# Performance work log

Measured on AMD Instinct MI355X. Metric: run time of the kernel, lower is better.

Reference implementation:

```python
import jax, jax.numpy as jnp
import numpy as np


def setup_inputs() -> dict:
    key = jax.random.key(0)
    k1, k2, k3 = jax.random.split(key, 3)
    B, S, E = 4, 4096, 512
    x = jax.random.normal(k1, (B, S, E), dtype=jnp.float32)
    # xavier_uniform for Linear weights; zero biases (per _reset_parameters)
    lim_qkv = float(np.sqrt(6.0 / (E + 3 * E)))
    W_qkv = jax.random.uniform(k2, (3 * E, E), minval=-lim_qkv, maxval=lim_qkv, dtype=jnp.float32)
    b_qkv = jnp.zeros((3 * E,), dtype=jnp.float32)
    lim_out = float(np.sqrt(6.0 / (E + E)))
    W_out = jax.random.uniform(k3, (E, E), minval=-lim_out, maxval=lim_out, dtype=jnp.float32)
    b_out = jnp.zeros((E,), dtype=jnp.float32)
    return {"x": x, "W_qkv": W_qkv, "b_qkv": b_qkv, "W_out": W_out, "b_out": b_out}


def reference(x, W_qkv, b_qkv, W_out, b_out):
    B, S, E = x.shape
    H = 8
    D = E // H
    qkv = x @ W_qkv.T + b_qkv                      # [B,S,3E]
    qkv = qkv.reshape(B, S, H, 3 * D)
    q, k, v = jnp.split(qkv, 3, axis=-1)            # each [B,S,H,D]
    q = jax.nn.sigmoid(q)
    k = jax.nn.sigmoid(k)
    # flow conservation normalizers (sum over seq dim=1, then feature dim=3)
    i = jnp.sum(q * jnp.sum(k, axis=1, keepdims=True), axis=3, keepdims=True)      # [B,S,H,1]
    o = jnp.sum(k * jnp.sum(q, axis=1, keepdims=True), axis=3, keepdims=True)
    i_hat = jnp.sum(q * jnp.sum(k / o, axis=1, keepdims=True), axis=3, keepdims=True)
    o_hat = jnp.sum(k * jnp.sum(q / i, axis=1, keepdims=True), axis=3, keepdims=True)
    # NOTE: faithful to source — matmul batches over (B,S) and contracts the HEAD axis
    vw = v * jax.nn.softmax(o_hat, axis=1)          # [B,S,H,D]
    kv = jnp.einsum('bshd,bshe->bsde', k, vw)       # [B,S,D,D]
    r = jnp.einsum('bshd,bsde->bshe', q / i, kv) * jax.nn.sigmoid(i_hat)  # [B,S,H,D]
    values = r.reshape(B, S, E)
    return values @ W_out.T + b_out
```

## Files before the change

kernel.cpp:

```cpp
#include <hip/hip_runtime.h>
#include <cstdint>
#include <cstddef>

#define B_ 4
#define S_ 4096
#define E_ 512
#define NPOS 16384
#define QKVC 1536
#define K_ 512

typedef unsigned short u16;
typedef u16    u16x8  __attribute__((ext_vector_type(8)));
typedef u16    u16x4  __attribute__((ext_vector_type(4)));
typedef __bf16 bf16x8 __attribute__((ext_vector_type(8)));
typedef float  f32x4  __attribute__((ext_vector_type(4)));

__device__ __forceinline__ u16 f2bf(float f) {
    unsigned u = __builtin_bit_cast(unsigned, f);
    unsigned r = (u + 0x7fffu + ((u >> 16) & 1u)) >> 16;
    return (u16)r;
}
__device__ __forceinline__ float bf2f(u16 u) {
    return __builtin_bit_cast(float, (unsigned)u << 16);
}
__device__ __forceinline__ float rcpf(float x) { return __builtin_amdgcn_rcpf(x); }

__device__ __forceinline__ void async16(const void* g, void* lds) {
    __builtin_amdgcn_global_load_lds(
        (const __attribute__((address_space(1))) unsigned int*)g,
        (__attribute__((address_space(3))) unsigned int*)lds, 16, 0, 0);
}

__global__ __launch_bounds__(256) void cvt3(
        const float4* __restrict__ x, const float4* __restrict__ wq, const float4* __restrict__ wo,
        u16x4* __restrict__ ox, u16x4* __restrict__ owq, u16x4* __restrict__ owo) {
    const int n1 = NPOS * E_ / 4, n2 = QKVC * E_ / 4, n3 = E_ * E_ / 4;
    int i = blockIdx.x * 256 + threadIdx.x;
    const float4* in; u16x4* out; int j;
    if (i < n1)            { in = x;  out = ox;  j = i; }
    else if (i < n1 + n2)  { in = wq; out = owq; j = i - n1; }
    else if (i < n1+n2+n3) { in = wo; out = owo; j = i - n1 - n2; }
    else return;
    float4 v = in[j];
    u16x4 o;
    o[0] = f2bf(v.x); o[1] = f2bf(v.y); o[2] = f2bf(v.z); o[3] = f2bf(v.w);
    out[j] = o;
}

__global__ __launch_bounds__(256) void gemm_qkv(
        const u16* __restrict__ A, const u16* __restrict__ Bw,
        const float* __restrict__ bias,
        u16* __restrict__ Qb, u16* __restrict__ Kb, u16* __restrict__ Vb,
        int K) {
    __shared__ u16 As[128 * 32];
    __shared__ u16 Bs[128 * 32];
    const int tid  = threadIdx.x;
    const int wave = tid >> 6, lane = tid & 63;
    const int m0 = blockIdx.y * 128, n0 = blockIdx.x * 128;
    const int wm = (wave & 1) * 64, wn = (wave >> 1) * 64;

    const int srow = wave * 16 + (lane >> 2);
    const int scol = (lane & 3) * 8;
    const u16* Ap = A  + (size_t)(m0 + srow) * K + scol;
    const u16* Bp = Bw + (size_t)(n0 + srow) * K + scol;
    u16* AsW = &As[wave * 512];
    u16* BsW = &Bs[wave * 512];
    const size_t rstep = (size_t)64 * K;

    f32x4 acc[4][4] = {};
    const int fr = lane & 15, fk = (lane >> 4) * 8;

    for (int k0 = 0; k0 < K; k0 += 32) {
        async16(Ap + k0,         AsW);
        async16(Ap + k0 + rstep, AsW + 2048);
        async16(Bp + k0,         BsW);
        async16(Bp + k0 + rstep, BsW + 2048);
        __syncthreads();
        bf16x8 a[4], b[4];
        #pragma unroll
        for (int i = 0; i < 4; ++i)
            a[i] = *(const bf16x8*)&As[(wm + i * 16 + fr) * 32 + fk];
        #pragma unroll
        for (int j = 0; j < 4; ++j)
            b[j] = *(const bf16x8*)&Bs[(wn + j * 16 + fr) * 32 + fk];
        #pragma unroll
        for (int i = 0; i < 4; ++i)
            #pragma unroll
            for (int j = 0; j < 4; ++j)
                acc[i][j] = __builtin_amdgcn_mfma_f32_16x16x32_bf16(a[i], b[j], acc[i][j], 0, 0, 0);
        __syncthreads();
    }

    const int cn = lane & 15, rb = (lane >> 4) * 4;
    const int cg   = (n0 + wn) >> 6;
    const int type = cg % 3;
    const int hb   = cg / 3;
    u16* dst = (type == 0) ? Qb : (type == 1) ? Kb : Vb;
    const bool sg = (type < 2);
    #pragma unroll
    for (int i = 0; i < 4; ++i) {
        int mbase = m0 + wm + i * 16 + rb;
        #pragma unroll
        for (int j = 0; j < 4; ++j) {
            int ccol = j * 16 + cn;
            float bv = bias[n0 + wn + ccol];
            int outcol = hb * 64 + ccol;
            f32x4 av = acc[i][j];
            #pragma unroll
            for (int r = 0; r < 4; ++r) {
                float v = av[r] + bv;
                if (sg) v = 1.f / (1.f + __expf(-v));
                dst[(size_t)(mbase + r) * 512 + outcol] = f2bf(v);
            }
        }
    }
}

__global__ __launch_bounds__(256) void gemm_out(
        const u16* __restrict__ A, const u16* __restrict__ Bw,
        const float* __restrict__ bias, float* __restrict__ C,
        int N, int K) {
    __shared__ u16 As[128 * 32];
    __shared__ u16 Bs[128 * 32];
    const int tid  = threadIdx.x;
    const int wave = tid >> 6, lane = tid & 63;
    const int m0 = blockIdx.y * 128, n0 = blockIdx.x * 128;
    const int wm = (wave & 1) * 64, wn = (wave >> 1) * 64;
    const int srow = wave * 16 + (lane >> 2);
    const int scol = (lane & 3) * 8;
    const u16* Ap = A  + (size_t)(m0 + srow) * K + scol;
    const u16* Bp = Bw + (size_t)(n0 + srow) * K + scol;
    u16* AsW = &As[wave * 512];
    u16* BsW = &Bs[wave * 512];
    const size_t rstep = (size_t)64 * K;
    f32x4 acc[4][4] = {};
    const int fr = lane & 15, fk = (lane >> 4) * 8;
    for (int k0 = 0; k0 < K; k0 += 32) {
        async16(Ap + k0,         AsW);
        async16(Ap + k0 + rstep, AsW + 2048);
        async16(Bp + k0,         BsW);
        async16(Bp + k0 + rstep, BsW + 2048);
        __syncthreads();
        bf16x8 a[4], b[4];
        #pragma unroll
        for (int i = 0; i < 4; ++i)
            a[i] = *(const bf16x8*)&As[(wm + i * 16 + fr) * 32 + fk];
        #pragma unroll
        for (int j = 0; j < 4; ++j)
            b[j] = *(const bf16x8*)&Bs[(wn + j * 16 + fr) * 32 + fk];
        #pragma unroll
        for (int i = 0; i < 4; ++i)
            #pragma unroll
            for (int j = 0; j < 4; ++j)
                acc[i][j] = __builtin_amdgcn_mfma_f32_16x16x32_bf16(a[i], b[j], acc[i][j], 0, 0, 0);
        __syncthreads();
    }
    const int cn = lane & 15, rb = (lane >> 4) * 4;
    #pragma unroll
    for (int i = 0; i < 4; ++i) {
        int mbase = m0 + wm + i * 16 + rb;
        #pragma unroll
        for (int j = 0; j < 4; ++j) {
            int nn = n0 + wn + j * 16 + cn;
            float bv = bias[nn];
            f32x4 av = acc[i][j];
            #pragma unroll
            for (int r = 0; r < 4; ++r)
                C[(size_t)(mbase + r) * N + nn] = av[r] + bv;
        }
    }
}

__global__ __launch_bounds__(256, 4) void sum_qk(
        const u16* __restrict__ Qg, const u16* __restrict__ Kg,
        float* __restrict__ part) {
    __shared__ float red[4][1024];
    const int blk = blockIdx.x;
    const int b = blk >> 8, chunk = blk & 255;
    const int w = threadIdx.x >> 6, lane = threadIdx.x & 63;
    const int p0 = b * S_ + chunk * 16 + w * 4;
    float aq[8] = {}, ak[8] = {};
    #pragma unroll
    for (int it = 0; it < 4; ++it) {
        size_t off = (size_t)(p0 + it) * 512 + lane * 8;
        u16x8 q8 = *(const u16x8*)(Qg + off);
        u16x8 k8 = *(const u16x8*)(Kg + off);
        #pragma unroll
        for (int j = 0; j < 8; ++j) { aq[j] += bf2f(q8[j]); ak[j] += bf2f(k8[j]); }
    }
    #pragma unroll
    for (int j = 0; j < 8; ++j) {
        red[w][lane * 8 + j]       = aq[j];
        red[w][512 + lane * 8 + j] = ak[j];
    }
    __syncthreads();
    const int tid = threadIdx.x;
    float* dst = part + (size_t)blk * 1024;
    #pragma unroll
    for (int rr = 0; rr < 4; ++rr) {
        int slot = rr * 256 + tid;
        dst[slot] = red[0][slot] + red[1][slot] + red[2][slot] + red[3][slot];
    }
}

__global__ __launch_bounds__(256) void fold_qk(
        const float* __restrict__ part, float* __restrict__ sumq, float* __restrict__ sumk) {
    int t = blockIdx.x * 256 + threadIdx.x;
    int b = t >> 10, slot = t & 1023;
    float a = 0.f;
    const float* p = part + (size_t)b * 256 * 1024 + slot;
    for (int c = 0; c < 256; ++c) a += p[(size_t)c * 1024];
    if (slot < 512) sumq[b * 512 + slot] = a;
    else            sumk[b * 512 + (slot - 512)] = a;
}

__global__ __launch_bounds__(256, 4) void p2_io(
        const u16* __restrict__ Qg, const u16* __restrict__ Kg,
        const float* __restrict__ sumq, const float* __restrict__ sumk,
        float* __restrict__ iv, float* __restrict__ part) {
    __shared__ float red[4][1024];
    const int blk = blockIdx.x;
    const int b = blk >> 9, chunk = blk & 511;
    const int w = threadIdx.x >> 6, lane = threadIdx.x & 63;
    const int p0 = b * S_ + chunk * 8 + w * 2;
    float skL[8], sqL[8];
    #pragma unroll
    for (int j = 0; j < 8; ++j) {
        skL[j] = sumk[b * 512 + lane * 8 + j];
        sqL[j] = sumq[b * 512 + lane * 8 + j];
    }
    float aqi[8] = {}, ako[8] = {};
    #pragma unroll
    for (int it = 0; it < 2; ++it) {
        int p = p0 + it;
        size_t off = (size_t)p * 512 + lane * 8;
        u16x8 q8 = *(const u16x8*)(Qg + off);
        u16x8 k8 = *(const u16x8*)(Kg + off);
        float qf[8], kf[8];
        #pragma unroll
        for (int j = 0; j < 8; ++j) { qf[j] = bf2f(q8[j]); kf[j] = bf2f(k8[j]); }
        float di = 0.f, dox = 0.f;
        #pragma unroll
        for (int j = 0; j < 8; ++j) { di += qf[j] * skL[j]; dox += kf[j] * sqL[j]; }
        di  += __shfl_xor(di, 1);  di  += __shfl_xor(di, 2);  di  += __shfl_xor(di, 4);
        dox += __shfl_xor(dox, 1); dox += __shfl_xor(dox, 2); dox += __shfl_xor(dox, 4);
        if ((lane & 7) == 0) iv[(size_t)p * 8 + (lane >> 3)] = di;
        float ri = rcpf(di), ro = rcpf(dox);
        #pragma unroll
        for (int j = 0; j < 8; ++j) { aqi[j] += qf[j] * ri; ako[j] += kf[j] * ro; }
    }
    #pragma unroll
    for (int j = 0; j < 8; ++j) {
        red[w][lane * 8 + j]       = aqi[j];
        red[w][512 + lane * 8 + j] = ako[j];
    }
    __syncthreads();
    const int tid = threadIdx.x;
    float* dst = part + (size_t)blk * 1024;
    #pragma unroll
    for (int rr = 0; rr < 4; ++rr) {
        int slot = rr * 256 + tid;
        dst[slot] = red[0][slot] + red[1][slot] + red[2][slot] + red[3][slot];
    }
}

__global__ __launch_bounds__(256) void fold_io(
        const float* __restrict__ part, float* __restrict__ sumqi, float* __restrict__ sumko) {
    int t = blockIdx.x * 256 + threadIdx.x;
    int b = t >> 10, slot = t & 1023;
    float a = 0.f;
    const float* p = part + (size_t)b * 512 * 1024 + slot;
    for (int c = 0; c < 512; ++c) a += p[(size_t)c * 1024];
    if (slot < 512) sumqi[b * 512 + slot] = a;
    else            sumko[b * 512 + (slot - 512)] = a;
}

__global__ __launch_bounds__(256, 4) void p3_io2(
        const u16* __restrict__ Qg, const u16* __restrict__ Kg,
        const float* __restrict__ sumqi, const float* __restrict__ sumko,
        const float* __restrict__ iv,
        float* __restrict__ rsc, float* __restrict__ wexp, float* __restrict__ smpart) {
    __shared__ float smr[4][8];
    const int blk = blockIdx.x;
    const int b = blk >> 9, chunk = blk & 511;
    const int w = threadIdx.x >> 6, lane = threadIdx.x & 63;
    const int p0 = b * S_ + chunk * 8 + w * 2;
    float skoL[8], sqiL[8];
    #pragma unroll
    for (int j = 0; j < 8; ++j) {
        skoL[j] = sumko[b * 512 + lane * 8 + j];
        sqiL[j] = sumqi[b * 512 + lane * 8 + j];
    }
    float smacc = 0.f;
    #pragma unroll
    for (int it = 0; it < 2; ++it) {
        int p = p0 + it;
        size_t off = (size_t)p * 512 + lane * 8;
        u16x8 q8 = *(const u16x8*)(Qg + off);
        u16x8 k8 = *(const u16x8*)(Kg + off);
        float dih = 0.f, doh = 0.f;
        #pragma unroll
        for (int j = 0; j < 8; ++j) {
            dih += bf2f(q8[j]) * skoL[j];
            doh += bf2f(k8[j]) * sqiL[j];
        }
        dih += __shfl_xor(dih, 1); dih += __shfl_xor(dih, 2); dih += __shfl_xor(dih, 4);
        doh += __shfl_xor(doh, 1); doh += __shfl_xor(doh, 2); doh += __shfl_xor(doh, 4);
        if ((lane & 7) == 0) {
            int h = lane >> 3;
            float sig = 1.f / (1.f + __expf(-dih));
            rsc[(size_t)p * 8 + h] = sig * rcpf(iv[(size_t)p * 8 + h]);
            float we = __expf(fminf(doh, 80.f));
            wexp[(size_t)p * 8 + h] = we;
            smacc += we;
        }
    }
    if ((lane & 7) == 0) smr[w][lane >> 3] = smacc;
    __syncthreads();
    if (threadIdx.x < 8)
        smpart[(size_t)blk * 8 + threadIdx.x] =
            smr[0][threadIdx.x] + smr[1][threadIdx.x] + smr[2][threadIdx.x] + smr[3][threadIdx.x];
}

__global__ __launch_bounds__(256) void fold_sm(const float* __restrict__ smpart, float* __restrict__ sm) {
    __shared__ float red[256];
    int bh = blockIdx.x;
    int b = bh >> 3, h = bh & 7;
    float a = 0.f;
    for (int c = threadIdx.x; c < 512; c += 256)
        a += smpart[((size_t)b * 512 + c) * 8 + h];
    red[threadIdx.x] = a;
    __syncthreads();
    for (int st = 128; st > 0; st >>= 1) {
        if (threadIdx.x < st) red[threadIdx.x] += red[threadIdx.x + st];
        __syncthreads();
    }
    if (threadIdx.x == 0) sm[bh] = red[0];
}

__global__ __launch_bounds__(256) void finalize_kernel(
        const u16* __restrict__ Qg, const u16* __restrict__ Kg, const u16* __restrict__ Vg,
        const float* __restrict__ rsc, const float* __restrict__ wexp, const float* __restrict__ sm,
        u16* __restrict__ Rg) {
    __shared__ float Ml[4][2][8][9];
    __shared__ float vw[4][2][8][68];
    const int w = threadIdx.x >> 6, lane = threadIdx.x & 63;
    const int pp = blockIdx.x * 8 + w * 2;
    const int b = pp >> 12;

    {
        int pl = (lane >> 3) & 1, hh = lane & 7, quad = lane >> 4;
        const u16* qa = Qg + (size_t)(pp + pl) * 512 + hh * 64 + quad * 8;
        const u16* ka = Kg + (size_t)(pp + pl) * 512 + hh * 64 + quad * 8;
        bf16x8 a0 = __builtin_bit_cast(bf16x8, *(const u16x8*)qa);
        bf16x8 a1 = __builtin_bit_cast(bf16x8, *(const u16x8*)(qa + 32));
        bf16x8 b0 = __builtin_bit_cast(bf16x8, *(const u16x8*)ka);
        bf16x8 b1 = __builtin_bit_cast(bf16x8, *(const u16x8*)(ka + 32));
        f32x4 accm = {0.f, 0.f, 0.f, 0.f};
        accm = __builtin_amdgcn_mfma_f32_16x16x32_bf16(a0, b0, accm, 0, 0, 0);
        accm = __builtin_amdgcn_mfma_f32_16x16x32_bf16(a1, b1, accm, 0, 0, 0);
        if (((lane >> 5) & 1) == ((lane >> 3) & 1)) {
            int plm = lane >> 5, hr = ((lane >> 4) & 1) * 4, h2 = lane & 7;
            #pragma unroll
            for (int r = 0; r < 4; ++r)
                Ml[w][plm][hr + r][h2] = accm[r] * rsc[(size_t)(pp + plm) * 8 + hr + r];
        }
    }
    {
        int hv = lane >> 3, e0 = (lane & 7) * 8;
        float invsm = rcpf(sm[b * 8 + hv]);
        #pragma unroll
        for (int pl = 0; pl < 2; ++pl) {
            u16x8 v8 = *(const u16x8*)(Vg + (size_t)(pp + pl) * 512 + lane * 8);
            float wgt = wexp[(size_t)(pp + pl) * 8 + hv] * invsm;
            f32x4 x0, x1;
            #pragma unroll
            for (int j = 0; j < 4; ++j) { x0[j] = bf2f(v8[j]) * wgt; x1[j] = bf2f(v8[4 + j]) * wgt; }
            *(f32x4*)&vw[w][pl][hv][e0]     = x0;
            *(f32x4*)&vw[w][pl][hv][e0 + 4] = x1;
        }
    }
    __syncthreads();
    {
        int pl = lane >> 5, idx = lane & 31, h = idx >> 2, eq = (idx & 3) * 16;
        float outv[16] = {};
        #pragma unroll
        for (int h2 = 0; h2 < 8; ++h2) {
            float m = Ml[w][pl][h][h2];
            #pragma unroll
            for (int c = 0; c < 4; ++c) {
                f32x4 vv = *(const f32x4*)&vw[w][pl][h2][eq + c * 4];
                #pragma unroll
                for (int j = 0; j < 4; ++j) outv[c * 4 + j] += m * vv[j];
            }
        }
        u16x8 o0, o1;
        #pragma unroll
        for (int j = 0; j < 8; ++j) { o0[j] = f2bf(outv[j]); o1[j] = f2bf(outv[8 + j]); }
        u16* dstp = Rg + (size_t)(pp + pl) * 512 + h * 64 + eq;
        *(u16x8*)dstp       = o0;
        *(u16x8*)(dstp + 8) = o1;
    }
}

extern "C" void kernel_launch(void* const* d_in, const int* in_sizes, int n_in,
                              void* d_out, int out_size, void* d_ws, size_t ws_size,
                              hipStream_t stream) {
    const float* x    = (const float*)d_in[0];
    const float* Wqkv = (const float*)d_in[1];
    const float* bqkv = (const float*)d_in[2];
    const float* Wout = (const float*)d_in[3];
    const float* bout = (const float*)d_in[4];
    float* out = (float*)d_out;
    char* ws = (char*)d_ws;

    constexpr size_t SZ_XBF  = (size_t)NPOS * E_ * 2;
    constexpr size_t SZ_WQBF = (size_t)QKVC * E_ * 2;
    constexpr size_t SZ_WOBF = (size_t)E_ * E_ * 2;
    constexpr size_t SZ_QKVB = (size_t)NPOS * E_ * 2;
    constexpr size_t SZ_SUM  = (size_t)B_ * 512 * 4;
    constexpr size_t SZ_V8   = (size_t)NPOS * 8 * 4;
    constexpr size_t SZ_PART = (size_t)2048 * 1024 * 4;

    size_t off = 0;
    u16*   xbf    = (u16*)(ws + off);   off += SZ_XBF;
    u16*   wqbf   = (u16*)(ws + off);   off += SZ_WQBF;
    u16*   wobf   = (u16*)(ws + off);   off += SZ_WOBF;
    u16*   Qb     = (u16*)(ws + off);   off += SZ_QKVB;
    u16*   Kb     = (u16*)(ws + off);   off += SZ_QKVB;
    u16*   Vb     = (u16*)(ws + off);   off += SZ_QKVB;
    float* sumq   = (float*)(ws + off); off += SZ_SUM;
    float* sumk   = (float*)(ws + off); off += SZ_SUM;
    float* sumqi  = (float*)(ws + off); off += SZ_SUM;
    float* sumko  = (float*)(ws + off); off += SZ_SUM;
    float* sm     = (float*)(ws + off); off += 256;
    float* iv     = (float*)(ws + off); off += SZ_V8;
    float* rsc    = (float*)(ws + off); off += SZ_V8;
    float* wexp   = (float*)(ws + off); off += SZ_V8;
    float* smpart = (float*)(ws + off); off += (size_t)2048 * 8 * 4;
    float* part   = (float*)(ws + off); off += SZ_PART;
    u16*   rbf    = xbf;

    {
        const int n4 = (NPOS * E_ + QKVC * E_ + E_ * E_) / 4;
        cvt3<<<(n4 + 255) / 256, 256, 0, stream>>>(
            (const float4*)x, (const float4*)Wqkv, (const float4*)Wout,
            (u16x4*)xbf, (u16x4*)wqbf, (u16x4*)wobf);
    }

    gemm_qkv<<<dim3(QKVC / 128, NPOS / 128), 256, 0, stream>>>(
        xbf, wqbf, bqkv, Qb, Kb, Vb, K_);

    sum_qk<<<1024, 256, 0, stream>>>(Qb, Kb, part);
    fold_qk<<<16, 256, 0, stream>>>(part, sumq, sumk);

    p2_io<<<2048, 256, 0, stream>>>(Qb, Kb, sumq, sumk, iv, part);
    fold_io<<<16, 256, 0, stream>>>(part, sumqi, sumko);

    p3_io2<<<2048, 256, 0, stream>>>(Qb, Kb, sumqi, sumko, iv, rsc, wexp, smpart);
    fold_sm<<<32, 256, 0, stream>>>(smpart, sm);

    finalize_kernel<<<2048, 256, 0, stream>>>(Qb, Kb, Vb, rsc, wexp, sm, rbf);

    gemm_out<<<dim3(E_ / 128, NPOS / 128), 256, 0, stream>>>(
        rbf, wobf, bout, out, E_, K_);
}
```

Baseline: 226.2 us.

## Fuse Q/K column sums into QKV GEMM epilogue and move i_hat into finalize

The QKV GEMM epilogue now reduces the sigmoid outputs per column and writes per-tile partial sums, and a small fold kernel replaces the separate sum_qk pass that re-read Q and K. The i_hat dot product and sigmoid scaling move into the finalize kernel, so p3 only reads K and the rsc buffer is dropped. LDS reads in both GEMMs use an XOR swizzle to cut bank conflicts, and fold_io spreads its reduction over more blocks. The costs are extra epilogue work and a block barrier in the GEMM, plus some added arithmetic in finalize.

```diff
diff --git a/kernel.cpp b/kernel.cpp
--- a/kernel.cpp
+++ b/kernel.cpp
@@ -51,16 +51,18 @@
         const u16* __restrict__ A, const u16* __restrict__ Bw,
         const float* __restrict__ bias,
         u16* __restrict__ Qb, u16* __restrict__ Kb, u16* __restrict__ Vb,
+        float* __restrict__ pgem,
         int K) {
     __shared__ u16 As[128 * 32];
     __shared__ u16 Bs[128 * 32];
+    __shared__ float csums[2][2][64];
     const int tid  = threadIdx.x;
     const int wave = tid >> 6, lane = tid & 63;
     const int m0 = blockIdx.y * 128, n0 = blockIdx.x * 128;
     const int wm = (wave & 1) * 64, wn = (wave >> 1) * 64;
 
     const int srow = wave * 16 + (lane >> 2);
-    const int scol = (lane & 3) * 8;
+    const int scol = (((lane & 3) ^ ((lane >> 2) & 3))) * 8;
     const u16* Ap = A  + (size_t)(m0 + srow) * K + scol;
     const u16* Bp = Bw + (size_t)(n0 + srow) * K + scol;
     u16* AsW = &As[wave * 512];
@@ -68,7 +70,8 @@
     const size_t rstep = (size_t)64 * K;
 
     f32x4 acc[4][4] = {};
-    const int fr = lane & 15, fk = (lane >> 4) * 8;
+    const int fr = lane & 15, fq = lane >> 4;
+    const int fkA = ((fq ^ (fr & 3))) * 8;
 
     for (int k0 = 0; k0 < K; k0 += 32) {
         async16(Ap + k0,         AsW);
@@ -79,10 +82,10 @@
         bf16x8 a[4], b[4];
         #pragma unroll
         for (int i = 0; i < 4; ++i)
-            a[i] = *(const bf16x8*)&As[(wm + i * 16 + fr) * 32 + fk];
+            a[i] = *(const bf16x8*)&As[(wm + i * 16 + fr) * 32 + fkA];
         #pragma unroll
         for (int j = 0; j < 4; ++j)
-            b[j] = *(const bf16x8*)&Bs[(wn + j * 16 + fr) * 32 + fk];
+            b[j] = *(const bf16x8*)&Bs[(wn + j * 16 + fr) * 32 + fkA];
         #pragma unroll
         for (int i = 0; i < 4; ++i)
             #pragma unroll
@@ -97,22 +100,56 @@
     const int hb   = cg / 3;
     u16* dst = (type == 0) ? Qb : (type == 1) ? Kb : Vb;
     const bool sg = (type < 2);
-    #pragma unroll
-    for (int i = 0; i < 4; ++i) {
-        int mbase = m0 + wm + i * 16 + rb;
-        #pragma unroll
-        for (int j = 0; j < 4; ++j) {
-            int ccol = j * 16 + cn;
-            float bv = bias[n0 + wn + ccol];
-            int outcol = hb * 64 + ccol;
+    float col4[4];
+    #pragma unroll
+    for (int j = 0; j < 4; ++j) {
+        int ccol = j * 16 + cn;
+        float bv = bias[n0 + wn + ccol];
+        int outcol = hb * 64 + ccol;
+        float csum = 0.f;
+        #pragma unroll
+        for (int i = 0; i < 4; ++i) {
+            int mbase = m0 + wm + i * 16 + rb;
             f32x4 av = acc[i][j];
             #pragma unroll
             for (int r = 0; r < 4; ++r) {
                 float v = av[r] + bv;
                 if (sg) v = 1.f / (1.f + __expf(-v));
+                csum += v;
                 dst[(size_t)(mbase + r) * 512 + outcol] = f2bf(v);
             }
         }
+        csum += __shfl_xor(csum, 16);
+        csum += __shfl_xor(csum, 32);
+        col4[j] = csum;
+    }
+    if (lane < 16) {
+        #pragma unroll
+        for (int j = 0; j < 4; ++j)
+            csums[wave >> 1][wave & 1][j * 16 + lane] = col4[j];
+    }
+    __syncthreads();
+    if (tid < 128) {
+        int half = tid >> 6, c6 = tid & 63;
+        float s = csums[half][0][c6] + csums[half][1][c6];
+        int cgb = blockIdx.x * 2 + half;
+        pgem[((size_t)cgb * 128 + blockIdx.y) * 64 + c6] = s;
+    }
+}
+
+__global__ __launch_bounds__(256) void fold_gemm(
+        const float* __restrict__ pgem, float* __restrict__ sumq, float* __restrict__ sumk) {
+    int type = blockIdx.x >> 2, b = blockIdx.x & 3;
+    float* dst = (type == 0) ? sumq : sumk;
+    #pragma unroll
+    for (int rep = 0; rep < 2; ++rep) {
+        int col = rep * 256 + threadIdx.x;
+        int hbq = col >> 6, c6 = col & 63;
+        int cg = hbq * 3 + type;
+        float a = 0.f;
+        for (int mt = 0; mt < 32; ++mt)
+            a += pgem[((size_t)cg * 128 + b * 32 + mt) * 64 + c6];
+        dst[b * 512 + col] = a;
     }
 }
 
@@ -127,14 +164,15 @@
     const int m0 = blockIdx.y * 128, n0 = blockIdx.x * 128;
     const int wm = (wave & 1) * 64, wn = (wave >> 1) * 64;
     const int srow = wave * 16 + (lane >> 2);
-    const int scol = (lane & 3) * 8;
+    const int scol = (((lane & 3) ^ ((lane >> 2) & 3))) * 8;
     const u16* Ap = A  + (size_t)(m0 + srow) * K + scol;
     const u16* Bp = Bw + (size_t)(n0 + srow) * K + scol;
     u16* AsW = &As[wave * 512];
     u16* BsW = &Bs[wave * 512];
     const size_t rstep = (size_t)64 * K;
     f32x4 acc[4][4] = {};
-    const int fr = lane & 15, fk = (lane >> 4) * 8;
+    const int fr = lane & 15, fq = lane >> 4;
+    const int fkA = ((fq ^ (fr & 3))) * 8;
     for (int k0 = 0; k0 < K; k0 += 32) {
         async16(Ap + k0,         AsW);
         async16(Ap + k0 + rstep, AsW + 2048);
@@ -144,10 +182,10 @@
         bf16x8 a[4], b[4];
         #pragma unroll
         for (int i = 0; i < 4; ++i)
-            a[i] = *(const bf16x8*)&As[(wm + i * 16 + fr) * 32 + fk];
+            a[i] = *(const bf16x8*)&As[(wm + i * 16 + fr) * 32 + fkA];
         #pragma unroll
         for (int j = 0; j < 4; ++j)
-            b[j] = *(const bf16x8*)&Bs[(wn + j * 16 + fr) * 32 + fk];
+            b[j] = *(const bf16x8*)&Bs[(wn + j * 16 + fr) * 32 + fkA];
         #pragma unroll
         for (int i = 0; i < 4; ++i)
             #pragma unroll
@@ -169,49 +207,6 @@
                 C[(size_t)(mbase + r) * N + nn] = av[r] + bv;
         }
     }
-}
-
-__global__ __launch_bounds__(256, 4) void sum_qk(
-        const u16* __restrict__ Qg, const u16* __restrict__ Kg,
-        float* __restrict__ part) {
-    __shared__ float red[4][1024];
-    const int blk = blockIdx.x;
-    const int b = blk >> 8, chunk = blk & 255;
-    const int w = threadIdx.x >> 6, lane = threadIdx.x & 63;
-    const int p0 = b * S_ + chunk * 16 + w * 4;
-    float aq[8] = {}, ak[8] = {};
-    #pragma unroll
-    for (int it = 0; it < 4; ++it) {
-        size_t off = (size_t)(p0 + it) * 512 + lane * 8;
-        u16x8 q8 = *(const u16x8*)(Qg + off);
-        u16x8 k8 = *(const u16x8*)(Kg + off);
-        #pragma unroll
-        for (int j = 0; j < 8; ++j) { aq[j] += bf2f(q8[j]); ak[j] += bf2f(k8[j]); }
-    }
-    #pragma unroll
-    for (int j = 0; j < 8; ++j) {
-        red[w][lane * 8 + j]       = aq[j];
-        red[w][512 + lane * 8 + j] = ak[j];
-    }
-    __syncthreads();
-    const int tid = threadIdx.x;
-    float* dst = part + (size_t)blk * 1024;
-    #pragma unroll
-    for (int rr = 0; rr < 4; ++rr) {
-        int slot = rr * 256 + tid;
-        dst[slot] = red[0][slot] + red[1][slot] + red[2][slot] + red[3][slot];
-    }
-}
-
-__global__ __launch_bounds__(256) void fold_qk(
-        const float* __restrict__ part, float* __restrict__ sumq, float* __restrict__ sumk) {
-    int t = blockIdx.x * 256 + threadIdx.x;
-    int b = t >> 10, slot = t & 1023;
-    float a = 0.f;
-    const float* p = part + (size_t)b * 256 * 1024 + slot;
-    for (int c = 0; c < 256; ++c) a += p[(size_t)c * 1024];
-    if (slot < 512) sumq[b * 512 + slot] = a;
-    else            sumk[b * 512 + (slot - 512)] = a;
 }
 
 __global__ __launch_bounds__(256, 4) void p2_io(
@@ -266,52 +261,47 @@
 
 __global__ __launch_bounds__(256) void fold_io(
         const float* __restrict__ part, float* __restrict__ sumqi, float* __restrict__ sumko) {
-    int t = blockIdx.x * 256 + threadIdx.x;
-    int b = t >> 10, slot = t & 1023;
+    __shared__ float red[4][64];
+    const int b = blockIdx.x >> 4, sgrp = blockIdx.x & 15;
+    const int sub = threadIdx.x >> 6, lane = threadIdx.x & 63;
     float a = 0.f;
-    const float* p = part + (size_t)b * 512 * 1024 + slot;
-    for (int c = 0; c < 512; ++c) a += p[(size_t)c * 1024];
-    if (slot < 512) sumqi[b * 512 + slot] = a;
-    else            sumko[b * 512 + (slot - 512)] = a;
-}
-
-__global__ __launch_bounds__(256, 4) void p3_io2(
-        const u16* __restrict__ Qg, const u16* __restrict__ Kg,
-        const float* __restrict__ sumqi, const float* __restrict__ sumko,
-        const float* __restrict__ iv,
-        float* __restrict__ rsc, float* __restrict__ wexp, float* __restrict__ smpart) {
+    for (int i = 0; i < 128; ++i) {
+        int c = sub + i * 4;
+        a += part[((size_t)(b * 512 + c)) * 1024 + sgrp * 64 + lane];
+    }
+    red[sub][lane] = a;
+    __syncthreads();
+    if (threadIdx.x < 64) {
+        float s = red[0][lane] + red[1][lane] + red[2][lane] + red[3][lane];
+        int slot = sgrp * 64 + lane;
+        if (slot < 512) sumqi[b * 512 + slot] = s;
+        else            sumko[b * 512 + (slot - 512)] = s;
+    }
+}
+
+__global__ __launch_bounds__(256, 4) void p3_ohat(
+        const u16* __restrict__ Kg, const float* __restrict__ sumqi,
+        float* __restrict__ wexp, float* __restrict__ smpart) {
     __shared__ float smr[4][8];
     const int blk = blockIdx.x;
     const int b = blk >> 9, chunk = blk & 511;
     const int w = threadIdx.x >> 6, lane = threadIdx.x & 63;
     const int p0 = b * S_ + chunk * 8 + w * 2;
-    float skoL[8], sqiL[8];
-    #pragma unroll
-    for (int j = 0; j < 8; ++j) {
-        skoL[j] = sumko[b * 512 + lane * 8 + j];
-        sqiL[j] = sumqi[b * 512 + lane * 8 + j];
-    }
+    float sqiL[8];
+    #pragma unroll
+    for (int j = 0; j < 8; ++j) sqiL[j] = sumqi[b * 512 + lane * 8 + j];
     float smacc = 0.f;
     #pragma unroll
     for (int it = 0; it < 2; ++it) {
         int p = p0 + it;
-        size_t off = (size_t)p * 512 + lane * 8;
-        u16x8 q8 = *(const u16x8*)(Qg + off);
-        u16x8 k8 = *(const u16x8*)(Kg + off);
-        float dih = 0.f, doh = 0.f;
-        #pragma unroll
-        for (int j = 0; j < 8; ++j) {
-            dih += bf2f(q8[j]) * skoL[j];
-            doh += bf2f(k8[j]) * sqiL[j];
-        }
-        dih += __shfl_xor(dih, 1); dih += __shfl_xor(dih, 2); dih += __shfl_xor(dih, 4);
+        u16x8 k8 = *(const u16x8*)(Kg + (size_t)p * 512 + lane * 8);
+        float doh = 0.f;
+        #pragma unroll
+        for (int j = 0; j < 8; ++j) doh += bf2f(k8[j]) * sqiL[j];
         doh += __shfl_xor(doh, 1); doh += __shfl_xor(doh, 2); doh += __shfl_xor(doh, 4);
         if ((lane & 7) == 0) {
-            int h = lane >> 3;
-            float sig = 1.f / (1.f + __expf(-dih));
-            rsc[(size_t)p * 8 + h] = sig * rcpf(iv[(size_t)p * 8 + h]);
             float we = __expf(fminf(doh, 80.f));
-            wexp[(size_t)p * 8 + h] = we;
+            wexp[(size_t)p * 8 + (lane >> 3)] = we;
             smacc += we;
         }
     }
@@ -340,7 +330,8 @@
 
 __global__ __launch_bounds__(256) void finalize_kernel(
         const u16* __restrict__ Qg, const u16* __restrict__ Kg, const u16* __restrict__ Vg,
-        const float* __restrict__ rsc, const float* __restrict__ wexp, const float* __restrict__ sm,
+        const float* __restrict__ sumko, const float* __restrict__ iv,
+        const float* __restrict__ wexp, const float* __restrict__ sm,
         u16* __restrict__ Rg) {
     __shared__ float Ml[4][2][8][9];
     __shared__ float vw[4][2][8][68];
@@ -348,48 +339,61 @@
     const int pp = blockIdx.x * 8 + w * 2;
     const int b = pp >> 12;
 
-    {
-        int pl = (lane >> 3) & 1, hh = lane & 7, quad = lane >> 4;
-        const u16* qa = Qg + (size_t)(pp + pl) * 512 + hh * 64 + quad * 8;
-        const u16* ka = Kg + (size_t)(pp + pl) * 512 + hh * 64 + quad * 8;
-        bf16x8 a0 = __builtin_bit_cast(bf16x8, *(const u16x8*)qa);
-        bf16x8 a1 = __builtin_bit_cast(bf16x8, *(const u16x8*)(qa + 32));
-        bf16x8 b0 = __builtin_bit_cast(bf16x8, *(const u16x8*)ka);
-        bf16x8 b1 = __builtin_bit_cast(bf16x8, *(const u16x8*)(ka + 32));
-        f32x4 accm = {0.f, 0.f, 0.f, 0.f};
-        accm = __builtin_amdgcn_mfma_f32_16x16x32_bf16(a0, b0, accm, 0, 0, 0);
-        accm = __builtin_amdgcn_mfma_f32_16x16x32_bf16(a1, b1, accm, 0, 0, 0);
-        if (((lane >> 5) & 1) == ((lane >> 3) & 1)) {
-            int plm = lane >> 5, hr = ((lane >> 4) & 1) * 4, h2 = lane & 7;
-            #pragma unroll
-            for (int r = 0; r < 4; ++r)
-                Ml[w][plm][hr + r][h2] = accm[r] * rsc[(size_t)(pp + plm) * 8 + hr + r];
-        }
+    const int pl = (lane >> 3) & 1, hh = lane & 7, quad = lane >> 4;
+    const u16* qa = Qg + (size_t)(pp + pl) * 512 + hh * 64 + quad * 8;
+    const u16* ka = Kg + (size_t)(pp + pl) * 512 + hh * 64 + quad * 8;
+    u16x8 qv0 = *(const u16x8*)qa;
+    u16x8 qv1 = *(const u16x8*)(qa + 32);
+    bf16x8 b0 = __builtin_bit_cast(bf16x8, *(const u16x8*)ka);
+    bf16x8 b1 = __builtin_bit_cast(bf16x8, *(const u16x8*)(ka + 32));
+    f32x4 accm = {0.f, 0.f, 0.f, 0.f};
+    accm = __builtin_amdgcn_mfma_f32_16x16x32_bf16(__builtin_bit_cast(bf16x8, qv0), b0, accm, 0, 0, 0);
+    accm = __builtin_amdgcn_mfma_f32_16x16x32_bf16(__builtin_bit_cast(bf16x8, qv1), b1, accm, 0, 0, 0);
+
+    const float* sko = sumko + b * 512 + hh * 64 + quad * 8;
+    float dp = 0.f;
+    #pragma unroll
+    for (int j = 0; j < 8; ++j)
+        dp += bf2f(qv0[j]) * sko[j] + bf2f(qv1[j]) * sko[32 + j];
+    dp += __shfl_xor(dp, 16);
+    dp += __shfl_xor(dp, 32);
+    float sig = 1.f / (1.f + __expf(-dp));
+    float myrsc = sig * rcpf(iv[(size_t)(pp + pl) * 8 + hh]);
+
+    const int plm = lane >> 5, hr = ((lane >> 4) & 1) * 4, h2c = lane & 7;
+    float rsc4[4];
+    #pragma unroll
+    for (int r = 0; r < 4; ++r)
+        rsc4[r] = __shfl(myrsc, plm * 8 + hr + r);
+    if (((lane >> 5) & 1) == ((lane >> 3) & 1)) {
+        #pragma unroll
+        for (int r = 0; r < 4; ++r)
+            Ml[w][plm][hr + r][h2c] = accm[r] * rsc4[r];
     }
     {
         int hv = lane >> 3, e0 = (lane & 7) * 8;
         float invsm = rcpf(sm[b * 8 + hv]);
         #pragma unroll
-        for (int pl = 0; pl < 2; ++pl) {
-            u16x8 v8 = *(const u16x8*)(Vg + (size_t)(pp + pl) * 512 + lane * 8);
-            float wgt = wexp[(size_t)(pp + pl) * 8 + hv] * invsm;
+        for (int plv = 0; plv < 2; ++plv) {
+            u16x8 v8 = *(const u16x8*)(Vg + (size_t)(pp + plv) * 512 + lane * 8);
+            float wgt = wexp[(size_t)(pp + plv) * 8 + hv] * invsm;
             f32x4 x0, x1;
             #pragma unroll
             for (int j = 0; j < 4; ++j) { x0[j] = bf2f(v8[j]) * wgt; x1[j] = bf2f(v8[4 + j]) * wgt; }
-            *(f32x4*)&vw[w][pl][hv][e0]     = x0;
-            *(f32x4*)&vw[w][pl][hv][e0 + 4] = x1;
+            *(f32x4*)&vw[w][plv][hv][e0]     = x0;
+            *(f32x4*)&vw[w][plv][hv][e0 + 4] = x1;
         }
     }
     __syncthreads();
     {
-        int pl = lane >> 5, idx = lane & 31, h = idx >> 2, eq = (idx & 3) * 16;
+        int plo = lane >> 5, idx = lane & 31, h = idx >> 2, eq = (idx & 3) * 16;
         float outv[16] = {};
         #pragma unroll
         for (int h2 = 0; h2 < 8; ++h2) {
-            float m = Ml[w][pl][h][h2];
+            float m = Ml[w][plo][h][h2];
             #pragma unroll
             for (int c = 0; c < 4; ++c) {
-                f32x4 vv = *(const f32x4*)&vw[w][pl][h2][eq + c * 4];
+                f32x4 vv = *(const f32x4*)&vw[w][plo][h2][eq + c * 4];
                 #pragma unroll
                 for (int j = 0; j < 4; ++j) outv[c * 4 + j] += m * vv[j];
             }
@@ -397,7 +401,7 @@
         u16x8 o0, o1;
         #pragma unroll
         for (int j = 0; j < 8; ++j) { o0[j] = f2bf(outv[j]); o1[j] = f2bf(outv[8 + j]); }
-        u16* dstp = Rg + (size_t)(pp + pl) * 512 + h * 64 + eq;
+        u16* dstp = Rg + (size_t)(pp + plo) * 512 + h * 64 + eq;
         *(u16x8*)dstp       = o0;
         *(u16x8*)(dstp + 8) = o1;
     }
@@ -420,6 +424,7 @@
     constexpr size_t SZ_QKVB = (size_t)NPOS * E_ * 2;
     constexpr size_t SZ_SUM  = (size_t)B_ * 512 * 4;
     constexpr size_t SZ_V8   = (size_t)NPOS * 8 * 4;
+    constexpr size_t SZ_PGEM = (size_t)24 * 128 * 64 * 4;
     constexpr size_t SZ_PART = (size_t)2048 * 1024 * 4;
 
     size_t off = 0;
@@ -435,9 +440,9 @@
     float* sumko  = (float*)(ws + off); off += SZ_SUM;
     float* sm     = (float*)(ws + off); off += 256;
     float* iv     = (float*)(ws + off); off += SZ_V8;
-    float* rsc    = (float*)(ws + off); off += SZ_V8;
     float* wexp   = (float*)(ws + off); off += SZ_V8;
     float* smpart = (float*)(ws + off); off += (size_t)2048 * 8 * 4;
+    float* pgem   = (float*)(ws + off); off += SZ_PGEM;
     float* part   = (float*)(ws + off); off += SZ_PART;
     u16*   rbf    = xbf;
 
@@ -449,18 +454,16 @@
     }
 
     gemm_qkv<<<dim3(QKVC / 128, NPOS / 128), 256, 0, stream>>>(
-        xbf, wqbf, bqkv, Qb, Kb, Vb, K_);
-
-    sum_qk<<<1024, 256, 0, stream>>>(Qb, Kb, part);
-    fold_qk<<<16, 256, 0, stream>>>(part, sumq, sumk);
+        xbf, wqbf, bqkv, Qb, Kb, Vb, pgem, K_);
+    fold_gemm<<<8, 256, 0, stream>>>(pgem, sumq, sumk);
 
     p2_io<<<2048, 256, 0, stream>>>(Qb, Kb, sumq, sumk, iv, part);
-    fold_io<<<16, 256, 0, stream>>>(part, sumqi, sumko);
-
-    p3_io2<<<2048, 256, 0, stream>>>(Qb, Kb, sumqi, sumko, iv, rsc, wexp, smpart);
+    fold_io<<<64, 256, 0, stream>>>(part, sumqi, sumko);
+
+    p3_ohat<<<2048, 256, 0, stream>>>(Kb, sumqi, wexp, smpart);
     fold_sm<<<32, 256, 0, stream>>>(smpart, sm);
 
-    finalize_kernel<<<2048, 256, 0, stream>>>(Qb, Kb, Vb, rsc, wexp, sm, rbf);
+    finalize_kernel<<<2048, 256, 0, stream>>>(Qb, Kb, Vb, sumko, iv, wexp, sm, rbf);
 
     gemm_out<<<dim3(E_ / 128, NPOS / 128), 256, 0, stream>>>(
         rbf, wobf, bout, out, E_, K_);
```

Result: faster. 201.8 us (-10.8%).
